# Kernel tuning notes

Hardware: AMD Instinct MI355X
Metric: run time of the kernel (lower is better)

The kernel has to match this reference:

```python
import jax, jax.numpy as jnp
import numpy as np

N, D, E, K = 16384, 4096, 128, 2

def setup_inputs() -> dict:
    key = jax.random.key(0)
    k1, k2 = jax.random.split(key)
    x = jax.random.normal(k1, (N, D), dtype=jnp.float32)
    W = jax.random.normal(k2, (E, D), dtype=jnp.float32) * (1.0 / np.sqrt(D))
    b = jnp.zeros((E,), dtype=jnp.float32)
    return {"x": x, "W": W, "b": b}

def reference(x, W, b):
    # logits = x @ W.T + b  -> [N, E]
    logits = jnp.einsum('nd,ed->ne', x, W) + b
    confidence = jax.nn.sigmoid(logits)
    top_k_vals, top_k_indices = jax.lax.top_k(confidence, K)  # [N, K]
    return top_k_vals, top_k_indices
```

## Files before the change

### kernel.cpp

```cpp
#include <hip/hip_runtime.h>
#include <stdint.h>
#include <math.h>

#define N_ROWS 16384
#define D_DIM  4096
#define E_EXP  128
#define BM     32
#define BKR    128
#define NR     (D_DIM / BKR)
#define TAU    2.5e-4f

typedef short  short8 __attribute__((ext_vector_type(8)));
typedef float  f32x4  __attribute__((ext_vector_type(4)));

__device__ __forceinline__ uint32_t bf16_rne(float f) {
  uint32_t u = __builtin_bit_cast(uint32_t, f);
  return (u + 0x7fffu + ((u >> 16) & 1u)) >> 16;
}

__global__ __launch_bounds__(256) void k0_split(const float* __restrict__ W,
                                                uint16_t* __restrict__ wt) {
  const int b  = blockIdx.x;
  const int t  = threadIdx.x;
  const int eg  = b >> 5;
  const int kcg = b & 31;
  const int kc  = kcg * 4 + (t >> 6);
  const int lane = t & 63;
  const int e  = eg * 16 + (lane & 15);
  const int k0 = kc * 32 + (lane >> 4) * 8;

  const float* src = W + (size_t)e * D_DIM + k0;
  f32x4 w0 = *(const f32x4*)src;
  f32x4 w1 = *(const f32x4*)(src + 4);
  float wf[8] = {w0[0], w0[1], w0[2], w0[3], w1[0], w1[1], w1[2], w1[3]};

  uint16_t h[8], l[8];
  #pragma unroll
  for (int j = 0; j < 8; ++j) {
    uint32_t hh = bf16_rne(wf[j]);
    float hf = __builtin_bit_cast(float, hh << 16);
    h[j] = (uint16_t)hh;
    l[j] = (uint16_t)bf16_rne(wf[j] - hf);
  }
  const size_t blkh = ((size_t)(eg * 128 + kc) * 2 + 0) * 512;
  const size_t blkl = ((size_t)(eg * 128 + kc) * 2 + 1) * 512;
  *(short8*)(wt + blkh + lane * 8) = *(const short8*)h;
  *(short8*)(wt + blkl + lane * 8) = *(const short8*)l;
}

__global__ __launch_bounds__(512, 4) void k1_main(
    const float* __restrict__ x, const uint16_t* __restrict__ wt,
    const float* __restrict__ bias, float* __restrict__ out, int* __restrict__ flags)
{
  __shared__ __align__(16) uint8_t smem[32768];
  float* Ld = (float*)smem;

  const int t    = threadIdx.x;
  const int lane = t & 63;
  const int wv   = __builtin_amdgcn_readfirstlane(t >> 6);
  const int row0 = blockIdx.x * BM;

  const int srow = t >> 4;
  const int skg  = t & 15;
  const float* xp = x + (size_t)(row0 + srow) * D_DIM + skg * 8;

  const int s_w = skg >> 2, gg_w = skg & 3, rr_w = srow & 15, rg_w = srow >> 4;
  const int p_w  = gg_w * 16 + (rr_w ^ (gg_w << 1) ^ s_w);
  const int wa_h = (s_w * 4 + rg_w * 2 + 0) * 1024 + p_w * 16;
  const int wa_l = wa_h + 1024;

  const int ggr = lane >> 4, rrr = lane & 15;
  const int p_r0 = ggr * 16 + (rrr ^ (ggr << 1));

  const short8* Wt8 = (const short8*)wt;
  const int ccol = lane & 15;

  f32x4 acc[2] = {};

  f32x4 xa0, xa1, xb0, xb1, xc0, xc1;
  xa0 = *((const f32x4*)xp + 0); xa1 = *((const f32x4*)xp + 1);
  xb0 = *((const f32x4*)(xp + BKR) + 0); xb1 = *((const f32x4*)(xp + BKR) + 1);
  xc0 = *((const f32x4*)(xp + 2 * BKR) + 0); xc1 = *((const f32x4*)(xp + 2 * BKR) + 1);

  #pragma unroll 2
  for (int r = 0; r < NR; ++r) {
    short8 Wc[8];
    {
      const size_t base = ((size_t)(wv * 128 + r * 4) * 2) * 64 + lane;
      #pragma unroll
      for (int s = 0; s < 4; ++s) {
        Wc[s * 2 + 0] = Wt8[base + (size_t)(s * 2 + 0) * 64];
        Wc[s * 2 + 1] = Wt8[base + (size_t)(s * 2 + 1) * 64];
      }
    }

    float xf[8] = {xa0[0], xa0[1], xa0[2], xa0[3], xa1[0], xa1[1], xa1[2], xa1[3]};
    uint32_t hpk[4], lpk[4];
    #pragma unroll
    for (int j = 0; j < 4; ++j) {
      uint32_t h0 = bf16_rne(xf[2*j]), h1 = bf16_rne(xf[2*j+1]);
      float h0f = __builtin_bit_cast(float, h0 << 16);
      float h1f = __builtin_bit_cast(float, h1 << 16);
      uint32_t l0 = bf16_rne(xf[2*j] - h0f), l1 = bf16_rne(xf[2*j+1] - h1f);
      hpk[j] = h0 | (h1 << 16);
      lpk[j] = l0 | (l1 << 16);
    }
    uint8_t* buf = smem + (r & 1) * 16384;
    *(uint4*)(buf + wa_h) = make_uint4(hpk[0], hpk[1], hpk[2], hpk[3]);
    *(uint4*)(buf + wa_l) = make_uint4(lpk[0], lpk[1], lpk[2], lpk[3]);

    xa0 = xb0; xa1 = xb1; xb0 = xc0; xb1 = xc1;
    if (r + 3 < NR) {
      const f32x4* np = (const f32x4*)(xp + (size_t)(r + 3) * BKR);
      xc0 = np[0]; xc1 = np[1];
    }

    asm volatile("s_waitcnt lgkmcnt(0)" ::: "memory");
    __builtin_amdgcn_s_barrier();

    #pragma unroll
    for (int s = 0; s < 4; ++s) {
      const int pr = p_r0 ^ s;
      const short8 bh = Wc[s * 2 + 0], bl = Wc[s * 2 + 1];
      #pragma unroll
      for (int rg = 0; rg < 2; ++rg) {
        const uint8_t* fb = buf + (s * 4 + rg * 2) * 1024 + pr * 16;
        short8 ah = *(const short8*)fb;
        short8 al = *(const short8*)(fb + 1024);
        acc[rg] = __builtin_amdgcn_mfma_f32_16x16x32_bf16(ah, bh, acc[rg], 0, 0, 0);
        acc[rg] = __builtin_amdgcn_mfma_f32_16x16x32_bf16(al, bh, acc[rg], 0, 0, 0);
        acc[rg] = __builtin_amdgcn_mfma_f32_16x16x32_bf16(ah, bl, acc[rg], 0, 0, 0);
      }
    }
  }

  float b0 = bias[wv * 16 + ccol];
  __syncthreads();
  #pragma unroll
  for (int rg = 0; rg < 2; ++rg)
    #pragma unroll
    for (int i = 0; i < 4; ++i) {
      int row = rg * 16 + ggr * 4 + i;
      int e = wv * 16 + ccol;
      Ld[row * 128 + e] = acc[rg][i] + b0;
    }
  __syncthreads();

  {
    const int row = t >> 4, part = t & 15;
    float l1 = -3e38f, l2 = -3e38f, l3 = -3e38f;
    int   i1 = -1, i2 = -1, i3 = -1;
    auto ins = [&](float v, int e) {
      if (v > l1 || (v == l1 && e < i1)) { l3=l2; i3=i2; l2=l1; i2=i1; l1=v; i1=e; }
      else if (v > l2 || (v == l2 && e < i2)) { l3=l2; i3=i2; l2=v; i2=e; }
      else if (v > l3 || (v == l3 && e < i3)) { l3=v; i3=e; }
    };
    #pragma unroll
    for (int j = 0; j < 2; ++j) {
      const float* pp = Ld + row * 128 + part * 8 + j * 4;
      f32x4 v = *(const f32x4*)pp;
      int eb = part * 8 + j * 4;
      ins(v[0], eb); ins(v[1], eb + 1); ins(v[2], eb + 2); ins(v[3], eb + 3);
    }
    #pragma unroll
    for (int m = 1; m <= 8; m <<= 1) {
      float a1 = __shfl_xor(l1, m), a2 = __shfl_xor(l2, m), a3 = __shfl_xor(l3, m);
      int   b1i = __shfl_xor(i1, m), b2i = __shfl_xor(i2, m), b3i = __shfl_xor(i3, m);
      ins(a1, b1i); ins(a2, b2i); ins(a3, b3i);
    }
    if (part == 0) {
      int grow = row0 + row;
      int fl = ((l1 - l2) < TAU) || ((l2 - l3) < TAU);
      flags[grow] = fl;
      out[(size_t)grow * 2 + 0] = 1.f / (1.f + __expf(-l1));
      out[(size_t)grow * 2 + 1] = 1.f / (1.f + __expf(-l2));
      out[(size_t)N_ROWS * 2 + (size_t)grow * 2 + 0] = (float)i1;
      out[(size_t)N_ROWS * 2 + (size_t)grow * 2 + 1] = (float)i2;
    }
  }
}

__global__ __launch_bounds__(1024) void k2_fix(
    const float* __restrict__ x, const float* __restrict__ W,
    const float* __restrict__ bias, const int* __restrict__ flags,
    float* __restrict__ out)
{
  __shared__ double lgs[E_EXP];
  const int t    = threadIdx.x;
  const int wvi  = t >> 6, lane = t & 63;
  const int e    = wvi * 8 + (lane >> 3);
  const int sub  = lane & 7;
  const int rbase = blockIdx.x * 8;

  for (int rr = 0; rr < 8; ++rr) {
    const int row = rbase + rr;
    if (!flags[row]) continue;
    const float* xr = x + (size_t)row * D_DIM;
    const float* wr = W + (size_t)e * D_DIM;
    double a0 = 0.0, a1 = 0.0, a2 = 0.0, a3 = 0.0;
    for (int j = 0; j < 128; ++j) {
      const int c4 = (j * 8 + sub) * 4;
      f32x4 xv = *(const f32x4*)(xr + c4);
      f32x4 wvv = *(const f32x4*)(wr + c4);
      a0 += (double)xv[0] * wvv[0];
      a1 += (double)xv[1] * wvv[1];
      a2 += (double)xv[2] * wvv[2];
      a3 += (double)xv[3] * wvv[3];
    }
    double acc = (a0 + a1) + (a2 + a3);
    #pragma unroll
    for (int m = 1; m <= 4; m <<= 1) acc += __shfl_xor(acc, m);
    if (sub == 0) lgs[e] = acc + (double)bias[e];
    __syncthreads();
    if (t == 0) {
      double l1 = -1e300, l2 = -1e300; int i1 = -1, i2 = -1;
      for (int ee = 0; ee < E_EXP; ++ee) {
        double v = lgs[ee];
        if (v > l1) { l2 = l1; i2 = i1; l1 = v; i1 = ee; }
        else if (v > l2) { l2 = v; i2 = ee; }
      }
      out[(size_t)row * 2 + 0] = (float)(1.0 / (1.0 + exp(-l1)));
      out[(size_t)row * 2 + 1] = (float)(1.0 / (1.0 + exp(-l2)));
      out[(size_t)N_ROWS * 2 + (size_t)row * 2 + 0] = (float)i1;
      out[(size_t)N_ROWS * 2 + (size_t)row * 2 + 1] = (float)i2;
    }
    __syncthreads();
  }
}

extern "C" void kernel_launch(void* const* d_in, const int* in_sizes, int n_in,
                              void* d_out, int out_size, void* d_ws, size_t ws_size,
                              hipStream_t stream) {
  const float* x  = (const float*)d_in[0];
  const float* Wm = (const float*)d_in[1];
  const float* b  = (const float*)d_in[2];
  float* out = (float*)d_out;

  uint16_t* wt = (uint16_t*)d_ws;
  int* flags = (int*)((uint8_t*)d_ws + 2u * 1024 * 1024);

  k0_split<<<dim3(256), dim3(256), 0, stream>>>(Wm, wt);
  k1_main<<<dim3(N_ROWS / BM), dim3(512), 0, stream>>>(x, wt, b, out, flags);
  k2_fix<<<dim3(N_ROWS / 8), dim3(1024), 0, stream>>>(x, Wm, b, flags, out);
}
```

Measured before the change: 171.3 us.

## Split GEMM K dimension across four blocks with separate reduce/top-k kernel

Splits the 4096-long reduction into four chunks, so the main kernel launches four times as many blocks, each writing fp32 partial logits to workspace. A new reduce kernel sums the partials, adds bias, and runs the top-k and flagging step. The aim is more parallelism and occupancy across the GPU's CUs (launch bounds raised to 8 waves-per-EU hint). In exchange it writes and reads back 32 MB of partials and adds one kernel launch.

```diff
diff --git a/kernel.cpp b/kernel.cpp
--- a/kernel.cpp
+++ b/kernel.cpp
@@ -7,7 +7,9 @@
 #define E_EXP  128
 #define BM     32
 #define BKR    128
-#define NR     (D_DIM / BKR)
+#define KSPLIT 4
+#define KCHUNK (D_DIM / KSPLIT)
+#define NR     (KCHUNK / BKR)
 #define TAU    2.5e-4f
 
 typedef short  short8 __attribute__((ext_vector_type(8)));
@@ -48,21 +50,24 @@
   *(short8*)(wt + blkl + lane * 8) = *(const short8*)l;
 }
 
-__global__ __launch_bounds__(512, 4) void k1_main(
+__global__ __launch_bounds__(512, 8) void k1_main(
     const float* __restrict__ x, const uint16_t* __restrict__ wt,
-    const float* __restrict__ bias, float* __restrict__ out, int* __restrict__ flags)
+    float* __restrict__ part)
 {
   __shared__ __align__(16) uint8_t smem[32768];
-  float* Ld = (float*)smem;
 
   const int t    = threadIdx.x;
   const int lane = t & 63;
   const int wv   = __builtin_amdgcn_readfirstlane(t >> 6);
-  const int row0 = blockIdx.x * BM;
+  const int bid  = blockIdx.x;
+  const int rt   = bid >> 2;
+  const int ks   = bid & 3;
+  const int row0 = rt * BM;
+  const int kb0  = ks * KCHUNK;
 
   const int srow = t >> 4;
   const int skg  = t & 15;
-  const float* xp = x + (size_t)(row0 + srow) * D_DIM + skg * 8;
+  const float* xp = x + (size_t)(row0 + srow) * D_DIM + kb0 + skg * 8;
 
   const int s_w = skg >> 2, gg_w = skg & 3, rr_w = srow & 15, rg_w = srow >> 4;
   const int p_w  = gg_w * 16 + (rr_w ^ (gg_w << 1) ^ s_w);
@@ -86,7 +91,7 @@
   for (int r = 0; r < NR; ++r) {
     short8 Wc[8];
     {
-      const size_t base = ((size_t)(wv * 128 + r * 4) * 2) * 64 + lane;
+      const size_t base = ((size_t)(wv * 128 + ks * 32 + r * 4) * 2) * 64 + lane;
       #pragma unroll
       for (int s = 0; s < 4; ++s) {
         Wc[s * 2 + 0] = Wt8[base + (size_t)(s * 2 + 0) * 64];
@@ -134,49 +139,61 @@
     }
   }
 
-  float b0 = bias[wv * 16 + ccol];
-  __syncthreads();
+  float* dst = part + ((size_t)ks * N_ROWS + row0) * E_EXP;
   #pragma unroll
   for (int rg = 0; rg < 2; ++rg)
     #pragma unroll
     for (int i = 0; i < 4; ++i) {
       int row = rg * 16 + ggr * 4 + i;
       int e = wv * 16 + ccol;
-      Ld[row * 128 + e] = acc[rg][i] + b0;
-    }
-  __syncthreads();
-
-  {
-    const int row = t >> 4, part = t & 15;
-    float l1 = -3e38f, l2 = -3e38f, l3 = -3e38f;
-    int   i1 = -1, i2 = -1, i3 = -1;
-    auto ins = [&](float v, int e) {
-      if (v > l1 || (v == l1 && e < i1)) { l3=l2; i3=i2; l2=l1; i2=i1; l1=v; i1=e; }
-      else if (v > l2 || (v == l2 && e < i2)) { l3=l2; i3=i2; l2=v; i2=e; }
-      else if (v > l3 || (v == l3 && e < i3)) { l3=v; i3=e; }
-    };
-    #pragma unroll
-    for (int j = 0; j < 2; ++j) {
-      const float* pp = Ld + row * 128 + part * 8 + j * 4;
-      f32x4 v = *(const f32x4*)pp;
-      int eb = part * 8 + j * 4;
-      ins(v[0], eb); ins(v[1], eb + 1); ins(v[2], eb + 2); ins(v[3], eb + 3);
-    }
-    #pragma unroll
-    for (int m = 1; m <= 8; m <<= 1) {
-      float a1 = __shfl_xor(l1, m), a2 = __shfl_xor(l2, m), a3 = __shfl_xor(l3, m);
-      int   b1i = __shfl_xor(i1, m), b2i = __shfl_xor(i2, m), b3i = __shfl_xor(i3, m);
-      ins(a1, b1i); ins(a2, b2i); ins(a3, b3i);
-    }
-    if (part == 0) {
-      int grow = row0 + row;
-      int fl = ((l1 - l2) < TAU) || ((l2 - l3) < TAU);
-      flags[grow] = fl;
-      out[(size_t)grow * 2 + 0] = 1.f / (1.f + __expf(-l1));
-      out[(size_t)grow * 2 + 1] = 1.f / (1.f + __expf(-l2));
-      out[(size_t)N_ROWS * 2 + (size_t)grow * 2 + 0] = (float)i1;
-      out[(size_t)N_ROWS * 2 + (size_t)grow * 2 + 1] = (float)i2;
-    }
+      dst[(size_t)row * E_EXP + e] = acc[rg][i];
+    }
+}
+
+__global__ __launch_bounds__(512) void k3_reduce(
+    const float* __restrict__ part, const float* __restrict__ bias,
+    float* __restrict__ out, int* __restrict__ flags)
+{
+  const int t = threadIdx.x;
+  const int row = t >> 4, prt = t & 15;
+  const int grow = blockIdx.x * 32 + row;
+  const float* pp = part + (size_t)grow * E_EXP + prt * 8;
+
+  f32x4 s0 = {}, s1 = {};
+  #pragma unroll
+  for (int ks = 0; ks < KSPLIT; ++ks) {
+    const float* q = pp + (size_t)ks * N_ROWS * E_EXP;
+    f32x4 a = *(const f32x4*)q;
+    f32x4 b = *(const f32x4*)(q + 4);
+    s0 += a; s1 += b;
+  }
+  float lv[8] = {s0[0], s0[1], s0[2], s0[3], s1[0], s1[1], s1[2], s1[3]};
+
+  float l1 = -3e38f, l2 = -3e38f, l3 = -3e38f;
+  int   i1 = -1, i2 = -1, i3 = -1;
+  auto ins = [&](float v, int e) {
+    if (v > l1 || (v == l1 && e < i1)) { l3=l2; i3=i2; l2=l1; i2=i1; l1=v; i1=e; }
+    else if (v > l2 || (v == l2 && e < i2)) { l3=l2; i3=i2; l2=v; i2=e; }
+    else if (v > l3 || (v == l3 && e < i3)) { l3=v; i3=e; }
+  };
+  #pragma unroll
+  for (int j = 0; j < 8; ++j) {
+    int e = prt * 8 + j;
+    ins(lv[j] + bias[e], e);
+  }
+  #pragma unroll
+  for (int m = 1; m <= 8; m <<= 1) {
+    float a1 = __shfl_xor(l1, m), a2 = __shfl_xor(l2, m), a3 = __shfl_xor(l3, m);
+    int   b1i = __shfl_xor(i1, m), b2i = __shfl_xor(i2, m), b3i = __shfl_xor(i3, m);
+    ins(a1, b1i); ins(a2, b2i); ins(a3, b3i);
+  }
+  if (prt == 0) {
+    int fl = ((l1 - l2) < TAU) || ((l2 - l3) < TAU);
+    flags[grow] = fl;
+    out[(size_t)grow * 2 + 0] = 1.f / (1.f + __expf(-l1));
+    out[(size_t)grow * 2 + 1] = 1.f / (1.f + __expf(-l2));
+    out[(size_t)N_ROWS * 2 + (size_t)grow * 2 + 0] = (float)i1;
+    out[(size_t)N_ROWS * 2 + (size_t)grow * 2 + 1] = (float)i2;
   }
 }
 
@@ -236,10 +253,12 @@
   const float* b  = (const float*)d_in[2];
   float* out = (float*)d_out;
 
-  uint16_t* wt = (uint16_t*)d_ws;
-  int* flags = (int*)((uint8_t*)d_ws + 2u * 1024 * 1024);
+  uint16_t* wt   = (uint16_t*)d_ws;
+  int*      flags = (int*)((uint8_t*)d_ws + 2u * 1024 * 1024);
+  float*    part = (float*)((uint8_t*)d_ws + 4u * 1024 * 1024);
 
   k0_split<<<dim3(256), dim3(256), 0, stream>>>(Wm, wt);
-  k1_main<<<dim3(N_ROWS / BM), dim3(512), 0, stream>>>(x, wt, b, out, flags);
+  k1_main<<<dim3((N_ROWS / BM) * KSPLIT), dim3(512), 0, stream>>>(x, wt, part);
+  k3_reduce<<<dim3(N_ROWS / 32), dim3(512), 0, stream>>>(part, b, out, flags);
   k2_fix<<<dim3(N_ROWS / 8), dim3(1024), 0, stream>>>(x, Wm, b, flags, out);
 }
```

Measured after the change: 430.4 us. 151% more time.
